# Performance work log

Measured on AMD Instinct MI355X. Metric: run time of the kernel, lower is better.

## Reference

```python
import jax, jax.numpy as jnp
import numpy as np

EPS = 1e-6

def _normalize(x):
    # x / sqrt(max(||x||^2, eps)) -- matches torch clamp_min on squared norm
    n2 = jnp.sum(x * x, axis=-1, keepdims=True)
    return x / jnp.sqrt(jnp.maximum(n2, EPS))

def setup_inputs() -> dict:
    key = jax.random.key(0)
    k1, k2, k3, k4 = jax.random.split(key, 4)
    B, N, M, D = 2, 4096, 4096, 256
    state_dim, out_dim = 2 * D, 512
    em1 = jax.random.normal(k1, (B, N, D), dtype=jnp.float32)
    em2 = jax.random.normal(k2, (B, M, D), dtype=jnp.float32)
    # fc params (torch Linear init: U(-1/sqrt(in), 1/sqrt(in)))
    bound = 1.0 / np.sqrt(state_dim)
    W = jax.random.uniform(k3, (out_dim, state_dim), minval=-bound, maxval=bound, dtype=jnp.float32)
    b = jax.random.uniform(k4, (out_dim,), minval=-bound, maxval=bound, dtype=jnp.float32)
    return {"em1": em1, "em2": em2, "W": W, "b": b}

def reference(em1, em2, W, b):
    # cosine similarity = normalized GEMM (same math as broadcast mul+sum)
    s = jnp.einsum('bnd,bmd->bnm', _normalize(em1), _normalize(em2))  # [B,N,M]
    soft = jax.nn.softmax(s, axis=-1)
    x = jnp.einsum('bnm,bmd->bnd', soft, em2)                          # [B,N,D]
    emb = jnp.concatenate([em1, x], axis=-1)                           # [B,N,2D]
    h = jax.nn.relu(emb @ W.T + b)                                     # [B,N,out_dim]
    return h
```

## Files before the change

### kernel.cpp

```cpp
#include <hip/hip_runtime.h>

#define BATCH 2
#define NQ    4096
#define MK    4096
#define DD    256
#define ODIM  512
#define SDIM  512
#define NROWS (BATCH * NQ)
#define BM    64
#define BK    64
#define MSPLIT 4
#define MCHUNK (MK / MSPLIT)
#define NKT    (MCHUNK / BK)
#define XSPLIT (BATCH * NQ * DD)

#define NCH_E1 (NROWS * DD / 8)
#define NCH_K  NCH_E1
#define NCH_V  NCH_E1
#define NCH_W  (ODIM * SDIM / 8)
#define RN_BLOCKS 4096

typedef short bf16x8 __attribute__((ext_vector_type(8)));
typedef float f32x16 __attribute__((ext_vector_type(16)));

__device__ __forceinline__ float bf2f(unsigned short h) {
    unsigned int u = ((unsigned int)h) << 16;
    float f;
    __builtin_memcpy(&f, &u, 4);
    return f;
}
__device__ __forceinline__ unsigned short f2bf(float f) {
    unsigned int u;
    __builtin_memcpy(&u, &f, 4);
    u = (u + 0x7FFFu + ((u >> 16) & 1u)) >> 16;
    return (unsigned short)u;
}
union frag_cast { uint4 u; bf16x8 b; unsigned short h[8]; };
__device__ __forceinline__ bf16x8 ldg_frag(const unsigned short* p) {
    frag_cast c;
    c.u = *(const uint4*)p;
    return c.b;
}
__device__ __forceinline__ void load_lds16(const unsigned short* g, unsigned short* l) {
    __builtin_amdgcn_global_load_lds(
        (const __attribute__((address_space(1))) void*)g,
        (__attribute__((address_space(3))) void*)l, 16, 0, 0);
}

__global__ void prep_kernel(const float* em1, const float* em2, const float* W,
                            float* rn, unsigned short* e1sw, unsigned short* ksw,
                            unsigned short* vsw, unsigned short* wsw) {
    int bid = blockIdx.x;
    if (bid < RN_BLOCKS) {
        int row  = bid * 4 + (threadIdx.x >> 6);
        int lane = threadIdx.x & 63;
        const float* src = (row < NROWS) ? em1 + (size_t)row * DD
                                         : em2 + (size_t)(row - NROWS) * DD;
        float4 v = *(const float4*)(src + lane * 4);
        float ss = v.x * v.x + v.y * v.y + v.z * v.z + v.w * v.w;
#pragma unroll
        for (int off = 1; off < 64; off <<= 1) ss += __shfl_xor(ss, off, 64);
        if (lane == 0) rn[row] = rsqrtf(fmaxf(ss, 1e-6f));
        return;
    }
    int cg = (bid - RN_BLOCKS) * 256 + threadIdx.x;
    if (cg < NCH_E1 + NCH_K) {
        const float* src;
        unsigned short* dst;
        int c0;
        if (cg < NCH_E1) { src = em1; dst = e1sw; c0 = cg; }
        else             { src = em2; dst = ksw;  c0 = cg - NCH_E1; }
        int g = c0 >> 10, c = c0 & 1023;
        int r31 = c & 31;
        int k0  = (c >> 5) * 8;
        const float* sp = src + (size_t)(g * 32 + r31) * DD + k0;
        float4 a = *(const float4*)sp;
        float4 b = *(const float4*)(sp + 4);
        ushort4 o1, o2;
        o1.x = f2bf(a.x); o1.y = f2bf(a.y); o1.z = f2bf(a.z); o1.w = f2bf(a.w);
        o2.x = f2bf(b.x); o2.y = f2bf(b.y); o2.z = f2bf(b.z); o2.w = f2bf(b.w);
        *(ushort4*)(dst + (size_t)c0 * 8)     = o1;
        *(ushort4*)(dst + (size_t)c0 * 8 + 4) = o2;
    } else if (cg < NCH_E1 + NCH_K + NCH_V) {
        int c0 = cg - (NCH_E1 + NCH_K);
        int b   = c0 >> 17;
        int r   = c0 & 131071;
        int dg  = r >> 14;
        int rr  = r & 16383;
        int oct = rr >> 5;
        int d31 = rr & 31;
        const float* sp = em2 + (size_t)(b * MK + oct * 8) * DD + dg * 32 + d31;
        ushort4 o1, o2;
        o1.x = f2bf(sp[0 * DD]); o1.y = f2bf(sp[1 * DD]);
        o1.z = f2bf(sp[2 * DD]); o1.w = f2bf(sp[3 * DD]);
        o2.x = f2bf(sp[4 * DD]); o2.y = f2bf(sp[5 * DD]);
        o2.z = f2bf(sp[6 * DD]); o2.w = f2bf(sp[7 * DD]);
        *(ushort4*)(vsw + (size_t)c0 * 8)     = o1;
        *(ushort4*)(vsw + (size_t)c0 * 8 + 4) = o2;
    } else {
        int c0 = cg - (NCH_E1 + NCH_K + NCH_V);
        if (c0 >= NCH_W) return;
        int g = c0 >> 11, c = c0 & 2047;
        int c31 = c & 31;
        int k0  = (c >> 5) * 8;
        const float* sp = W + (size_t)(g * 32 + c31) * SDIM + k0;
        float4 a = *(const float4*)sp;
        float4 b = *(const float4*)(sp + 4);
        ushort4 o1, o2;
        o1.x = f2bf(a.x); o1.y = f2bf(a.y); o1.z = f2bf(a.z); o1.w = f2bf(a.w);
        o2.x = f2bf(b.x); o2.y = f2bf(b.y); o2.z = f2bf(b.z); o2.w = f2bf(b.w);
        *(ushort4*)(wsw + (size_t)c0 * 8)     = o1;
        *(ushort4*)(wsw + (size_t)c0 * 8 + 4) = o2;
    }
}

__global__ __launch_bounds__(256, 2)
void flash_kernel(const unsigned short* e1sw, const unsigned short* ksw,
                  const unsigned short* vsw, const float* rn,
                  unsigned short* Xp, float* lbuf) {
    __shared__ unsigned short Ks[16384];
    __shared__ unsigned short Vs[16384];
    __shared__ unsigned short Ps[BM * 72];
    __shared__ float ls[2][BM];
    int tid = threadIdx.x, lane = tid & 63, w = tid >> 6;
    int l31 = lane & 31, lhalf = lane >> 5;
    int wr = w & 1, wc = w >> 1;
    int bid    = blockIdx.x;
    int mchunk = bid & 3;
    int rowblk = bid >> 2;
    int batch  = rowblk >> 6;
    int r0     = rowblk * BM;

    const unsigned short* qbase =
        e1sw + (size_t)(rowblk * 2 + wr) * 8192 + lhalf * 256 + l31 * 8;
    bf16x8 qf[16];
#pragma unroll
    for (int s = 0; s < 16; s++) qf[s] = ldg_frag(qbase + s * 512);

    float rqv[16];
#pragma unroll
    for (int i = 0; i < 16; i++) {
        int m = (i & 3) + 8 * (i >> 2) + 4 * lhalf;
        rqv[i] = rn[r0 + wr * 32 + m];
    }
    const float* rnk = rn + NROWS + batch * MK + mchunk * MCHUNK;

    const unsigned short* kchunk = ksw + (size_t)(batch * 128 + mchunk * 32) * 8192;
    const unsigned short* vbase  = vsw + (size_t)batch * 1048576 +
                                   (size_t)(mchunk * 128) * 256;

    f32x16 xacc[4];
#pragma unroll
    for (int t = 0; t < 4; t++)
#pragma unroll
        for (int i = 0; i < 16; i++) xacc[t][i] = 0.f;
    float lpart[16];
#pragma unroll
    for (int i = 0; i < 16; i++) lpart[i] = 0.f;

    for (int kt = 0; kt < NKT; kt++) {
        __syncthreads();
        {
            const unsigned short* ksrc = kchunk + (size_t)kt * 16384;
#pragma unroll
            for (int it = 0; it < 8; it++)
                load_lds16(ksrc + it * 2048 + tid * 8, &Ks[it * 2048 + tid * 8]);
            const unsigned short* vsrc = vbase + (size_t)(kt * 8) * 256;
#pragma unroll
            for (int dg = 0; dg < 8; dg++)
                load_lds16(vsrc + (size_t)dg * 131072 + tid * 8, &Vs[dg * 2048 + tid * 8]);
        }
        __syncthreads();
        f32x16 sA, sB;
#pragma unroll
        for (int i = 0; i < 16; i++) { sA[i] = 0.f; sB[i] = 0.f; }
        const unsigned short* kb = &Ks[wc * 8192 + lhalf * 256 + l31 * 8];
#pragma unroll
        for (int s = 0; s < 16; s += 2) {
            bf16x8 b0 = ldg_frag(kb + s * 512);
            bf16x8 b1 = ldg_frag(kb + (s + 1) * 512);
            sA = __builtin_amdgcn_mfma_f32_32x32x16_bf16(qf[s],     b0, sA, 0, 0, 0);
            sB = __builtin_amdgcn_mfma_f32_32x32x16_bf16(qf[s + 1], b1, sB, 0, 0, 0);
        }
        float rk = rnk[kt * BK + wc * 32 + l31];
#pragma unroll
        for (int i = 0; i < 16; i++) {
            float p = __expf((sA[i] + sB[i]) * rqv[i] * rk - 1.0f);
            unsigned short pb = f2bf(p);
            lpart[i] += bf2f(pb);
            int m = wr * 32 + (i & 3) + 8 * (i >> 2) + 4 * lhalf;
            Ps[m * 72 + wc * 32 + l31] = pb;
        }
        __syncthreads();
#pragma unroll
        for (int ks = 0; ks < 4; ks++) {
            frag_cast ac;
            ac.u = *(const uint4*)&Ps[(wr * 32 + l31) * 72 + ks * 16 + lhalf * 8];
#pragma unroll
            for (int nt = 0; nt < 4; nt++) {
                bf16x8 bf = ldg_frag(&Vs[((wc * 4 + nt) * 8 + ks * 2 + lhalf) * 256 + l31 * 8]);
                xacc[nt] = __builtin_amdgcn_mfma_f32_32x32x16_bf16(ac.b, bf, xacc[nt], 0, 0, 0);
            }
        }
    }

#pragma unroll
    for (int i = 0; i < 16; i++) {
        float v = lpart[i];
#pragma unroll
        for (int off = 1; off < 32; off <<= 1) v += __shfl_xor(v, off, 64);
        if (l31 == 0) {
            int m = wr * 32 + (i & 3) + 8 * (i >> 2) + 4 * lhalf;
            ls[wc][m] = v;
        }
    }
    __syncthreads();
    if (tid < BM)
        lbuf[(size_t)mchunk * NROWS + r0 + tid] = ls[0][tid] + ls[1][tid];

    unsigned short* xout = Xp + (size_t)mchunk * XSPLIT +
                           (size_t)(rowblk * 2 + wr) * 8192;
#pragma unroll
    for (int nt = 0; nt < 4; nt++) {
        int dcol = wc * 128 + nt * 32 + l31;
        int cbase = (dcol >> 3) * 256 + (dcol & 7);
#pragma unroll
        for (int i = 0; i < 16; i++) {
            int m = (i & 3) + 8 * (i >> 2) + 4 * lhalf;
            xout[cbase + m * 8] = f2bf(xacc[nt][i]);
        }
    }
}

__global__ __launch_bounds__(256, 4)
void final_gemm(const unsigned short* e1sw, const unsigned short* Xp,
                const float* lbuf, const unsigned short* wsw, const float* bias,
                float* out) {
    int tid = threadIdx.x, lane = tid & 63, w = tid >> 6;
    int l31 = lane & 31, lhalf = lane >> 5;
    int wr = w & 1, wc = w >> 1;
    int bid = blockIdx.x;
    int cb = bid & 7, rb = bid >> 3;
    int gA = rb * 2 + wr;
    int gB = cb * 2 + wc;

    int rowm = gA * 32 + l31;
    float l = lbuf[rowm] + lbuf[NROWS + rowm] +
              lbuf[2 * NROWS + rowm] + lbuf[3 * NROWS + rowm];
    float rinv = 1.0f / l;

    f32x16 acc;
#pragma unroll
    for (int i = 0; i < 16; i++) acc[i] = 0.f;

    const unsigned short* abase = e1sw + (size_t)gA * 8192 + lhalf * 256 + l31 * 8;
    const unsigned short* xbase = Xp   + (size_t)gA * 8192 + lhalf * 256 + l31 * 8;
    const unsigned short* bbase = wsw  + (size_t)gB * 16384 + lhalf * 256 + l31 * 8;

    for (int kk = 0; kk < 32; kk++) {
        bf16x8 afr;
        if (kk < 16) {
            afr = ldg_frag(abase + kk * 512);
        } else {
            const unsigned short* xp = xbase + (kk - 16) * 512;
            frag_cast p0, p1, p2, p3, u;
            p0.u = *(const uint4*)xp;
            p1.u = *(const uint4*)(xp + (size_t)XSPLIT);
            p2.u = *(const uint4*)(xp + 2 * (size_t)XSPLIT);
            p3.u = *(const uint4*)(xp + 3 * (size_t)XSPLIT);
#pragma unroll
            for (int j = 0; j < 8; j++) {
                float f = bf2f(p0.h[j]) + bf2f(p1.h[j]) +
                          bf2f(p2.h[j]) + bf2f(p3.h[j]);
                u.h[j] = f2bf(f * rinv);
            }
            afr = u.b;
        }
        bf16x8 bfr = ldg_frag(bbase + kk * 512);
        acc = __builtin_amdgcn_mfma_f32_32x32x16_bf16(afr, bfr, acc, 0, 0, 0);
    }

    int col = gB * 32 + l31;
    float bb = bias[col];
#pragma unroll
    for (int i = 0; i < 16; i++) {
        int row = gA * 32 + (i & 3) + 8 * (i >> 2) + 4 * lhalf;
        float v = acc[i] + bb;
        v = v > 0.f ? v : 0.f;
        out[(size_t)row * ODIM + col] = v;
    }
}

extern "C" void kernel_launch(void* const* d_in, const int* in_sizes, int n_in,
                              void* d_out, int out_size, void* d_ws, size_t ws_size,
                              hipStream_t stream) {
    const float* em1  = (const float*)d_in[0];
    const float* em2  = (const float*)d_in[1];
    const float* W    = (const float*)d_in[2];
    const float* bias = (const float*)d_in[3];
    float* out = (float*)d_out;

    char* ws = (char*)d_ws;
    unsigned short* e1sw = (unsigned short*)ws;
    unsigned short* ksw  = e1sw + (size_t)NROWS * DD;
    unsigned short* vsw  = ksw  + (size_t)NROWS * DD;
    unsigned short* wsw  = vsw  + (size_t)BATCH * DD * MK;
    unsigned short* Xp   = wsw  + (size_t)ODIM * SDIM;
    float* lbuf = (float*)(Xp + 4 * (size_t)XSPLIT);
    float* rn   = lbuf + 4 * (size_t)NROWS;

    const int swz_blocks = (NCH_E1 + NCH_K + NCH_V + NCH_W + 255) / 256;
    prep_kernel<<<RN_BLOCKS + swz_blocks, 256, 0, stream>>>(
        em1, em2, W, rn, e1sw, ksw, vsw, wsw);
    flash_kernel<<<(NROWS / BM) * MSPLIT, 256, 0, stream>>>(e1sw, ksw, vsw, rn, Xp, lbuf);
    final_gemm<<<(NROWS / 64) * (ODIM / 64), 256, 0, stream>>>(
        e1sw, Xp, lbuf, wsw, bias, out);
}
```

Measured before the change: 157.5 us.

## Software-pipeline flash loop, read V directly from global, and add split-reduce kernel

```diff
diff --git a/kernel.cpp b/kernel.cpp
--- a/kernel.cpp
+++ b/kernel.cpp
@@ -119,7 +119,6 @@
                   const unsigned short* vsw, const float* rn,
                   unsigned short* Xp, float* lbuf) {
     __shared__ unsigned short Ks[16384];
-    __shared__ unsigned short Vs[16384];
     __shared__ unsigned short Ps[BM * 72];
     __shared__ float ls[2][BM];
     int tid = threadIdx.x, lane = tid & 63, w = tid >> 6;
@@ -158,19 +157,26 @@
 #pragma unroll
     for (int i = 0; i < 16; i++) lpart[i] = 0.f;
 
+#pragma unroll
+    for (int it = 0; it < 8; it++)
+        load_lds16(kchunk + it * 2048 + tid * 8, &Ks[it * 2048 + tid * 8]);
+
     for (int kt = 0; kt < NKT; kt++) {
         __syncthreads();
-        {
-            const unsigned short* ksrc = kchunk + (size_t)kt * 16384;
-#pragma unroll
-            for (int it = 0; it < 8; it++)
-                load_lds16(ksrc + it * 2048 + tid * 8, &Ks[it * 2048 + tid * 8]);
-            const unsigned short* vsrc = vbase + (size_t)(kt * 8) * 256;
-#pragma unroll
-            for (int dg = 0; dg < 8; dg++)
-                load_lds16(vsrc + (size_t)dg * 131072 + tid * 8, &Vs[dg * 2048 + tid * 8]);
-        }
-        __syncthreads();
+        if (kt > 0) {
+            const unsigned short* vp = vbase + (size_t)((kt - 1) * 8) * 256 +
+                                       lhalf * 256 + l31 * 8;
+#pragma unroll
+            for (int ks = 0; ks < 4; ks++) {
+                frag_cast ac;
+                ac.u = *(const uint4*)&Ps[(wr * 32 + l31) * 72 + ks * 16 + lhalf * 8];
+#pragma unroll
+                for (int nt = 0; nt < 4; nt++) {
+                    bf16x8 bf = ldg_frag(vp + (size_t)(wc * 4 + nt) * 131072 + ks * 512);
+                    xacc[nt] = __builtin_amdgcn_mfma_f32_32x32x16_bf16(ac.b, bf, xacc[nt], 0, 0, 0);
+                }
+            }
+        }
         f32x16 sA, sB;
 #pragma unroll
         for (int i = 0; i < 16; i++) { sA[i] = 0.f; sB[i] = 0.f; }
@@ -183,6 +189,14 @@
             sB = __builtin_amdgcn_mfma_f32_32x32x16_bf16(qf[s + 1], b1, sB, 0, 0, 0);
         }
         float rk = rnk[kt * BK + wc * 32 + l31];
+        __syncthreads();
+        {
+            int ktn = (kt + 1 < NKT) ? kt + 1 : kt;
+            const unsigned short* ksrc = kchunk + (size_t)ktn * 16384;
+#pragma unroll
+            for (int it = 0; it < 8; it++)
+                load_lds16(ksrc + it * 2048 + tid * 8, &Ks[it * 2048 + tid * 8]);
+        }
 #pragma unroll
         for (int i = 0; i < 16; i++) {
             float p = __expf((sA[i] + sB[i]) * rqv[i] * rk - 1.0f);
@@ -191,14 +205,18 @@
             int m = wr * 32 + (i & 3) + 8 * (i >> 2) + 4 * lhalf;
             Ps[m * 72 + wc * 32 + l31] = pb;
         }
-        __syncthreads();
+    }
+    __syncthreads();
+    {
+        const unsigned short* vp = vbase + (size_t)((NKT - 1) * 8) * 256 +
+                                   lhalf * 256 + l31 * 8;
 #pragma unroll
         for (int ks = 0; ks < 4; ks++) {
             frag_cast ac;
             ac.u = *(const uint4*)&Ps[(wr * 32 + l31) * 72 + ks * 16 + lhalf * 8];
 #pragma unroll
             for (int nt = 0; nt < 4; nt++) {
-                bf16x8 bf = ldg_frag(&Vs[((wc * 4 + nt) * 8 + ks * 2 + lhalf) * 256 + l31 * 8]);
+                bf16x8 bf = ldg_frag(vp + (size_t)(wc * 4 + nt) * 131072 + ks * 512);
                 xacc[nt] = __builtin_amdgcn_mfma_f32_32x32x16_bf16(ac.b, bf, xacc[nt], 0, 0, 0);
             }
         }
@@ -232,50 +250,49 @@
     }
 }
 
+__global__ void reduce_kernel(const unsigned short* Xp, const float* lbuf,
+                              unsigned short* xnsw) {
+    int cg  = blockIdx.x * 256 + threadIdx.x;
+    int row = (cg >> 10) * 32 + (cg & 31);
+    float l = lbuf[row] + lbuf[NROWS + row] +
+              lbuf[2 * NROWS + row] + lbuf[3 * NROWS + row];
+    float rinv = 1.0f / l;
+    const unsigned short* p = Xp + (size_t)cg * 8;
+    frag_cast p0, p1, p2, p3, u;
+    p0.u = *(const uint4*)p;
+    p1.u = *(const uint4*)(p + (size_t)XSPLIT);
+    p2.u = *(const uint4*)(p + 2 * (size_t)XSPLIT);
+    p3.u = *(const uint4*)(p + 3 * (size_t)XSPLIT);
+#pragma unroll
+    for (int j = 0; j < 8; j++) {
+        float f = bf2f(p0.h[j]) + bf2f(p1.h[j]) + bf2f(p2.h[j]) + bf2f(p3.h[j]);
+        u.h[j] = f2bf(f * rinv);
+    }
+    *(uint4*)(xnsw + (size_t)cg * 8) = u.u;
+}
+
 __global__ __launch_bounds__(256, 4)
-void final_gemm(const unsigned short* e1sw, const unsigned short* Xp,
-                const float* lbuf, const unsigned short* wsw, const float* bias,
-                float* out) {
+void final_gemm(const unsigned short* e1sw, const unsigned short* xnsw,
+                const unsigned short* wsw, const float* bias, float* out) {
     int tid = threadIdx.x, lane = tid & 63, w = tid >> 6;
     int l31 = lane & 31, lhalf = lane >> 5;
     int wr = w & 1, wc = w >> 1;
     int bid = blockIdx.x;
-    int cb = bid & 7, rb = bid >> 3;
+    int rb = bid & 127, cb = bid >> 7;
     int gA = rb * 2 + wr;
     int gB = cb * 2 + wc;
 
-    int rowm = gA * 32 + l31;
-    float l = lbuf[rowm] + lbuf[NROWS + rowm] +
-              lbuf[2 * NROWS + rowm] + lbuf[3 * NROWS + rowm];
-    float rinv = 1.0f / l;
-
     f32x16 acc;
 #pragma unroll
     for (int i = 0; i < 16; i++) acc[i] = 0.f;
 
     const unsigned short* abase = e1sw + (size_t)gA * 8192 + lhalf * 256 + l31 * 8;
-    const unsigned short* xbase = Xp   + (size_t)gA * 8192 + lhalf * 256 + l31 * 8;
+    const unsigned short* xbase = xnsw + (size_t)gA * 8192 + lhalf * 256 + l31 * 8;
     const unsigned short* bbase = wsw  + (size_t)gB * 16384 + lhalf * 256 + l31 * 8;
 
     for (int kk = 0; kk < 32; kk++) {
-        bf16x8 afr;
-        if (kk < 16) {
-            afr = ldg_frag(abase + kk * 512);
-        } else {
-            const unsigned short* xp = xbase + (kk - 16) * 512;
-            frag_cast p0, p1, p2, p3, u;
-            p0.u = *(const uint4*)xp;
-            p1.u = *(const uint4*)(xp + (size_t)XSPLIT);
-            p2.u = *(const uint4*)(xp + 2 * (size_t)XSPLIT);
-            p3.u = *(const uint4*)(xp + 3 * (size_t)XSPLIT);
-#pragma unroll
-            for (int j = 0; j < 8; j++) {
-                float f = bf2f(p0.h[j]) + bf2f(p1.h[j]) +
-                          bf2f(p2.h[j]) + bf2f(p3.h[j]);
-                u.h[j] = f2bf(f * rinv);
-            }
-            afr = u.b;
-        }
+        bf16x8 afr = (kk < 16) ? ldg_frag(abase + kk * 512)
+                               : ldg_frag(xbase + (kk - 16) * 512);
         bf16x8 bfr = ldg_frag(bbase + kk * 512);
         acc = __builtin_amdgcn_mfma_f32_32x32x16_bf16(afr, bfr, acc, 0, 0, 0);
     }
@@ -306,13 +323,15 @@
     unsigned short* vsw  = ksw  + (size_t)NROWS * DD;
     unsigned short* wsw  = vsw  + (size_t)BATCH * DD * MK;
     unsigned short* Xp   = wsw  + (size_t)ODIM * SDIM;
-    float* lbuf = (float*)(Xp + 4 * (size_t)XSPLIT);
+    unsigned short* xnsw = Xp   + 4 * (size_t)XSPLIT;
+    float* lbuf = (float*)(xnsw + (size_t)NROWS * DD);
     float* rn   = lbuf + 4 * (size_t)NROWS;
 
     const int swz_blocks = (NCH_E1 + NCH_K + NCH_V + NCH_W + 255) / 256;
     prep_kernel<<<RN_BLOCKS + swz_blocks, 256, 0, stream>>>(
         em1, em2, W, rn, e1sw, ksw, vsw, wsw);
     flash_kernel<<<(NROWS / BM) * MSPLIT, 256, 0, stream>>>(e1sw, ksw, vsw, rn, Xp, lbuf);
+    reduce_kernel<<<NCH_E1 / 256, 256, 0, stream>>>(Xp, lbuf, xnsw);
     final_gemm<<<(NROWS / 64) * (ODIM / 64), 256, 0, stream>>>(
-        e1sw, Xp, lbuf, wsw, bias, out);
-}
+        e1sw, xnsw, wsw, bias, out);
+}
```

New measurement: 158.9 us. Within noise of the previous version (+0.9%).
